# Performance work log

Hardware: AMD Instinct MI355X
Metric: run time of the kernel (lower is better)

## Reference

```python
import jax, jax.numpy as jnp
import numpy as np

F = 192  # channels
HW = 8   # spatial map side


def _conv1x1(x, W, b):
    # x: [B,H,W,C], W: [C,C], b: [C] -- 1x1 conv == per-pixel matmul
    return jnp.einsum('bhwc,cd->bhwd', x, W) + b


def setup_inputs() -> dict:
    key = jax.random.key(0)
    ks = jax.random.split(key, 10)
    B = 4096
    s = 1.0 / np.sqrt(F)
    x = jax.random.normal(ks[0], (B, HW, HW, F), dtype=jnp.float32)
    Wf = jax.random.normal(ks[1], (F, F), dtype=jnp.float32) * s
    bf = jnp.zeros((F,), dtype=jnp.float32)
    Wg = jax.random.normal(ks[2], (F, F), dtype=jnp.float32) * s
    bg = jnp.zeros((F,), dtype=jnp.float32)
    Wh = jax.random.normal(ks[3], (F, F), dtype=jnp.float32) * s
    bh = jnp.zeros((F,), dtype=jnp.float32)
    Wo = jax.random.normal(ks[4], (F, F), dtype=jnp.float32) * s
    bo = jnp.zeros((F,), dtype=jnp.float32)
    # original initializes gamma to zero; use a small nonzero value so the
    # attention branch contributes to the output/gradients
    gamma = jnp.full((1, 1, 1), 0.1, dtype=jnp.float32)
    return {"x": x, "Wf": Wf, "bf": bf, "Wg": Wg, "bg": bg,
            "Wh": Wh, "bh": bh, "Wo": Wo, "bo": bo, "gamma": gamma}


def reference(x, Wf, bf, Wg, bg, Wh, bh, Wo, bo, gamma):
    B = x.shape[0]
    N = HW * HW  # 64 spatial positions
    fx = _conv1x1(x, Wf, bf).reshape(B, N, F)           # queries [B,N,F]
    gx = _conv1x1(x, Wg, bg)                            # [B,H,W,F]
    # tf.transpose to [B,F,H,W] then reshape -> [B,F,N]
    gx = jnp.transpose(gx, (0, 3, 1, 2)).reshape(B, F, N)
    attn = jax.nn.softmax(jnp.einsum('bnf,bfm->bnm', fx, gx), axis=-1)  # [B,N,N]
    hx = _conv1x1(x, Wh, bh).reshape(B, N, F)           # values [B,N,F]
    second = jnp.einsum('bnm,bmf->bnf', attn, hx).reshape(B, HW, HW, F)
    second = _conv1x1(second, Wo, bo)
    return x + gamma * second
```

## Files before the change

### kernel.cpp

```cpp
#include <hip/hip_runtime.h>

#define FCH 192
#define NPOS 64
#define PX 200
#define PH 72
#define PP 72

typedef float f32x4 __attribute__((ext_vector_type(4)));
typedef float float4_t __attribute__((ext_vector_type(4)));
typedef __bf16 bf16x8 __attribute__((ext_vector_type(8)));
typedef unsigned short ushort8_t __attribute__((ext_vector_type(8)));
typedef unsigned short ushort4_t __attribute__((ext_vector_type(4)));

__device__ __forceinline__ unsigned short f2bf(float f) {
  unsigned u = __builtin_bit_cast(unsigned, f);
  u += 0x7fffu + ((u >> 16) & 1u);
  return (unsigned short)(u >> 16);
}

__device__ __forceinline__ bf16x8 frag_ld(const unsigned short* p) {
  return __builtin_bit_cast(bf16x8, *(const ushort8_t*)p);
}

__global__ void prep_weights(const float* __restrict__ Wf, const float* __restrict__ Wg,
                             const float* __restrict__ Wh, const float* __restrict__ Wo,
                             unsigned short* __restrict__ wt) {
  int t = blockIdx.x * blockDim.x + threadIdx.x;
  int n = t % 192;
  int kb = (t / 192) % 48;
  int m = t / (192 * 48);
  const float* W = (m == 0) ? Wf : (m == 1) ? Wg : (m == 2) ? Wh : Wo;
  ushort4_t v;
#pragma unroll
  for (int i = 0; i < 4; ++i) v[i] = f2bf(W[(kb * 4 + i) * 192 + n]);
  *(ushort4_t*)(wt + ((size_t)(m * 192 + n) * 192 + kb * 4)) = v;
}

__global__ __launch_bounds__(256) void spatial_attn(
    const float* __restrict__ x, const unsigned short* __restrict__ wt,
    const float* __restrict__ bfv, const float* __restrict__ bgv,
    const float* __restrict__ bhv, const float* __restrict__ bov,
    const float* __restrict__ gamma_p, float* __restrict__ out) {
  __shared__ unsigned short lds[56832];
  unsigned short* sX  = lds;
  unsigned short* sF  = lds + 12800;
  unsigned short* sG  = lds + 25600;
  unsigned short* sHT = lds + 38400;
  unsigned short* sP  = lds + 52224;
  unsigned short* sS  = lds;

  const int b    = blockIdx.x;
  const int tid  = threadIdx.x;
  const int lane = tid & 63;
  const int w    = tid >> 6;
  const int l15  = lane & 15;
  const int l4   = lane >> 4;

  const float* xb = x + (size_t)b * (NPOS * FCH);

#pragma unroll
  for (int r = 0; r < 12; ++r) {
    int i = tid + 256 * r;
    float4_t v = *(const float4_t*)(xb + (size_t)i * 4);
    int row = (i * 4) / FCH, col = (i * 4) % FCH;
    ushort4_t u;
#pragma unroll
    for (int q = 0; q < 4; ++q) u[q] = f2bf(v[q]);
    *(ushort4_t*)(sX + row * PX + col) = u;
  }
  __syncthreads();

  const unsigned short* WfT = wt;
  const unsigned short* WgT = wt + 36864;
  const unsigned short* WhT = wt + 73728;
  const unsigned short* WoT = wt + 110592;

  auto conv_T = [&](const unsigned short* WT, const float* bias, unsigned short* dst) {
    f32x4 acc[3][4];
#pragma unroll
    for (int mt = 0; mt < 3; ++mt)
#pragma unroll
      for (int nt = 0; nt < 4; ++nt) acc[mt][nt] = f32x4{0.f, 0.f, 0.f, 0.f};
#pragma unroll
    for (int kk = 0; kk < 6; ++kk) {
      int kb = kk * 32 + l4 * 8;
      bf16x8 a[3], bb[4];
#pragma unroll
      for (int mt = 0; mt < 3; ++mt)
        a[mt] = frag_ld(WT + (size_t)(w * 48 + mt * 16 + l15) * 192 + kb);
#pragma unroll
      for (int nt = 0; nt < 4; ++nt)
        bb[nt] = frag_ld(sX + (nt * 16 + l15) * PX + kb);
#pragma unroll
      for (int mt = 0; mt < 3; ++mt)
#pragma unroll
        for (int nt = 0; nt < 4; ++nt)
          acc[mt][nt] = __builtin_amdgcn_mfma_f32_16x16x32_bf16(a[mt], bb[nt], acc[mt][nt], 0, 0, 0);
    }
#pragma unroll
    for (int mt = 0; mt < 3; ++mt) {
      int fb = w * 48 + mt * 16 + l4 * 4;
      float b0 = bias[fb], b1 = bias[fb + 1], b2 = bias[fb + 2], b3 = bias[fb + 3];
#pragma unroll
      for (int nt = 0; nt < 4; ++nt) {
        int n = nt * 16 + l15;
        ushort4_t u;
        u[0] = f2bf(acc[mt][nt][0] + b0);
        u[1] = f2bf(acc[mt][nt][1] + b1);
        u[2] = f2bf(acc[mt][nt][2] + b2);
        u[3] = f2bf(acc[mt][nt][3] + b3);
        *(ushort4_t*)(dst + n * PX + fb) = u;
      }
    }
  };
  conv_T(WfT, bfv, sF);
  conv_T(WgT, bgv, sG);

  {
    f32x4 acc[4][3];
#pragma unroll
    for (int mt = 0; mt < 4; ++mt)
#pragma unroll
      for (int nt = 0; nt < 3; ++nt) acc[mt][nt] = f32x4{0.f, 0.f, 0.f, 0.f};
#pragma unroll
    for (int kk = 0; kk < 6; ++kk) {
      int kb = kk * 32 + l4 * 8;
      bf16x8 a[4], bb[3];
#pragma unroll
      for (int mt = 0; mt < 4; ++mt)
        a[mt] = frag_ld(sX + (mt * 16 + l15) * PX + kb);
#pragma unroll
      for (int nt = 0; nt < 3; ++nt)
        bb[nt] = frag_ld(WhT + (size_t)(w * 48 + nt * 16 + l15) * 192 + kb);
#pragma unroll
      for (int mt = 0; mt < 4; ++mt)
#pragma unroll
        for (int nt = 0; nt < 3; ++nt)
          acc[mt][nt] = __builtin_amdgcn_mfma_f32_16x16x32_bf16(a[mt], bb[nt], acc[mt][nt], 0, 0, 0);
    }
#pragma unroll
    for (int mt = 0; mt < 4; ++mt) {
      int nb = mt * 16 + l4 * 4;
#pragma unroll
      for (int nt = 0; nt < 3; ++nt) {
        int f = w * 48 + nt * 16 + l15;
        float bv = bhv[f];
        ushort4_t u;
#pragma unroll
        for (int j = 0; j < 4; ++j) u[j] = f2bf(acc[mt][nt][j] + bv);
        *(ushort4_t*)(sHT + f * PH + nb) = u;
      }
    }
  }
  __syncthreads();

  {
    f32x4 lg[4];
#pragma unroll
    for (int mt = 0; mt < 4; ++mt) lg[mt] = f32x4{0.f, 0.f, 0.f, 0.f};
#pragma unroll
    for (int kk = 0; kk < 6; ++kk) {
      int kb = kk * 32 + l4 * 8;
      bf16x8 bb = frag_ld(sF + (w * 16 + l15) * PX + kb);
#pragma unroll
      for (int mt = 0; mt < 4; ++mt) {
        bf16x8 a = frag_ld(sG + (mt * 16 + l15) * PX + kb);
        lg[mt] = __builtin_amdgcn_mfma_f32_16x16x32_bf16(a, bb, lg[mt], 0, 0, 0);
      }
    }
    float mx = -1e30f;
#pragma unroll
    for (int mt = 0; mt < 4; ++mt)
#pragma unroll
      for (int j = 0; j < 4; ++j) mx = fmaxf(mx, lg[mt][j]);
    mx = fmaxf(mx, __shfl_xor(mx, 16));
    mx = fmaxf(mx, __shfl_xor(mx, 32));
    float p[4][4];
    float s = 0.f;
#pragma unroll
    for (int mt = 0; mt < 4; ++mt)
#pragma unroll
      for (int j = 0; j < 4; ++j) {
        p[mt][j] = exp2f((lg[mt][j] - mx) * 1.44269504f);
        s += p[mt][j];
      }
    s += __shfl_xor(s, 16);
    s += __shfl_xor(s, 32);
    float inv = 1.0f / s;
    int n = w * 16 + l15;
#pragma unroll
    for (int mt = 0; mt < 4; ++mt) {
      ushort4_t u;
#pragma unroll
      for (int j = 0; j < 4; ++j) u[j] = f2bf(p[mt][j] * inv);
      *(ushort4_t*)(sP + n * PP + mt * 16 + l4 * 4) = u;
    }
  }
  __syncthreads();

  {
    f32x4 acc[3][4];
#pragma unroll
    for (int mt = 0; mt < 3; ++mt)
#pragma unroll
      for (int nt = 0; nt < 4; ++nt) acc[mt][nt] = f32x4{0.f, 0.f, 0.f, 0.f};
#pragma unroll
    for (int kk = 0; kk < 2; ++kk) {
      int kb = kk * 32 + l4 * 8;
      bf16x8 a[3], bb[4];
#pragma unroll
      for (int mt = 0; mt < 3; ++mt)
        a[mt] = frag_ld(sHT + (w * 48 + mt * 16 + l15) * PH + kb);
#pragma unroll
      for (int nt = 0; nt < 4; ++nt)
        bb[nt] = frag_ld(sP + (nt * 16 + l15) * PP + kb);
#pragma unroll
      for (int mt = 0; mt < 3; ++mt)
#pragma unroll
        for (int nt = 0; nt < 4; ++nt)
          acc[mt][nt] = __builtin_amdgcn_mfma_f32_16x16x32_bf16(a[mt], bb[nt], acc[mt][nt], 0, 0, 0);
    }
#pragma unroll
    for (int mt = 0; mt < 3; ++mt) {
      int fb = w * 48 + mt * 16 + l4 * 4;
#pragma unroll
      for (int nt = 0; nt < 4; ++nt) {
        int n = nt * 16 + l15;
        ushort4_t u;
#pragma unroll
        for (int j = 0; j < 4; ++j) u[j] = f2bf(acc[mt][nt][j]);
        *(ushort4_t*)(sS + n * PX + fb) = u;
      }
    }
  }
  __syncthreads();

  {
    f32x4 acc[4][3];
#pragma unroll
    for (int mt = 0; mt < 4; ++mt)
#pragma unroll
      for (int nt = 0; nt < 3; ++nt) acc[mt][nt] = f32x4{0.f, 0.f, 0.f, 0.f};
#pragma unroll
    for (int kk = 0; kk < 6; ++kk) {
      int kb = kk * 32 + l4 * 8;
      bf16x8 a[4], bb[3];
#pragma unroll
      for (int mt = 0; mt < 4; ++mt)
        a[mt] = frag_ld(sS + (mt * 16 + l15) * PX + kb);
#pragma unroll
      for (int nt = 0; nt < 3; ++nt)
        bb[nt] = frag_ld(WoT + (size_t)(w * 48 + nt * 16 + l15) * 192 + kb);
#pragma unroll
      for (int mt = 0; mt < 4; ++mt)
#pragma unroll
        for (int nt = 0; nt < 3; ++nt)
          acc[mt][nt] = __builtin_amdgcn_mfma_f32_16x16x32_bf16(a[mt], bb[nt], acc[mt][nt], 0, 0, 0);
    }
    float gm = gamma_p[0];
    float* ob = out + (size_t)b * (NPOS * FCH);
#pragma unroll
    for (int nt = 0; nt < 3; ++nt) {
      int d = w * 48 + nt * 16 + l15;
      float bv = bov[d];
#pragma unroll
      for (int mt = 0; mt < 4; ++mt) {
        int nb = mt * 16 + l4 * 4;
#pragma unroll
        for (int j = 0; j < 4; ++j) {
          int idx = (nb + j) * FCH + d;
          ob[idx] = xb[idx] + gm * (acc[mt][nt][j] + bv);
        }
      }
    }
  }
}

extern "C" void kernel_launch(void* const* d_in, const int* in_sizes, int n_in,
                              void* d_out, int out_size, void* d_ws, size_t ws_size,
                              hipStream_t stream) {
  const float* x   = (const float*)d_in[0];
  const float* Wf  = (const float*)d_in[1];
  const float* bf_ = (const float*)d_in[2];
  const float* Wg  = (const float*)d_in[3];
  const float* bg_ = (const float*)d_in[4];
  const float* Wh  = (const float*)d_in[5];
  const float* bh_ = (const float*)d_in[6];
  const float* Wo  = (const float*)d_in[7];
  const float* bo_ = (const float*)d_in[8];
  const float* gm  = (const float*)d_in[9];
  unsigned short* wt = (unsigned short*)d_ws;

  prep_weights<<<144, 256, 0, stream>>>(Wf, Wg, Wh, Wo, wt);
  spatial_attn<<<4096, 256, 0, stream>>>(x, wt, bf_, bg_, bh_, bo_, gm, (float*)d_out);
}
```

Before: 561.9 us.

## Fold query/key and value/output weight products to remove two per-pixel GEMMs

Precomputes A = Wf·Wgᵀ and C2 = Wh·Wo, plus bias vectors, in small prep kernels. Bias terms that are constant along the softmax axis are dropped, and bh·Wo+bo is folded into a constant because attention rows sum to one. Per sample the kernel then runs two 64x192x192 projections instead of four. The block grows to 512 threads with smaller LDS to raise occupancy, and the output epilogue becomes a coalesced float4 residual add. Rounding the fused weight matrices to bf16 changes the numerics slightly.

```diff
diff --git a/kernel.cpp b/kernel.cpp
--- a/kernel.cpp
+++ b/kernel.cpp
@@ -17,52 +17,83 @@
   u += 0x7fffu + ((u >> 16) & 1u);
   return (unsigned short)(u >> 16);
 }
-
+__device__ __forceinline__ float bf2f(unsigned short s) {
+  unsigned u = ((unsigned)s) << 16;
+  return __builtin_bit_cast(float, u);
+}
 __device__ __forceinline__ bf16x8 frag_ld(const unsigned short* p) {
   return __builtin_bit_cast(bf16x8, *(const ushort8_t*)p);
 }
 
-__global__ void prep_weights(const float* __restrict__ Wf, const float* __restrict__ Wg,
-                             const float* __restrict__ Wh, const float* __restrict__ Wo,
-                             unsigned short* __restrict__ wt) {
+__global__ void prep_mats(const float* __restrict__ Wf, const float* __restrict__ Wg,
+                          const float* __restrict__ Wh, const float* __restrict__ Wo,
+                          unsigned short* __restrict__ AT, unsigned short* __restrict__ C2T) {
+  __shared__ float col[192];
+  int r = blockIdx.x;
+  int t = threadIdx.x;
+  if (r < 192) {
+    col[t] = Wg[r * 192 + t];
+    __syncthreads();
+    float acc = 0.f;
+#pragma unroll 4
+    for (int f = 0; f < 192; ++f) acc += Wf[t * 192 + f] * col[f];
+    AT[r * 192 + t] = f2bf(acc);
+  } else {
+    int d = r - 192;
+    col[t] = Wo[t * 192 + d];
+    __syncthreads();
+    float acc = 0.f;
+#pragma unroll 4
+    for (int f = 0; f < 192; ++f) acc += Wh[t * 192 + f] * col[f];
+    C2T[d * 192 + t] = f2bf(acc);
+  }
+}
+
+__global__ void prep_vecs(const float* __restrict__ Wg, const float* __restrict__ bfv,
+                          const float* __restrict__ Wo, const float* __restrict__ bhv,
+                          const float* __restrict__ bov,
+                          float* __restrict__ vg, float* __restrict__ c0) {
   int t = blockIdx.x * blockDim.x + threadIdx.x;
-  int n = t % 192;
-  int kb = (t / 192) % 48;
-  int m = t / (192 * 48);
-  const float* W = (m == 0) ? Wf : (m == 1) ? Wg : (m == 2) ? Wh : Wo;
-  ushort4_t v;
-#pragma unroll
-  for (int i = 0; i < 4; ++i) v[i] = f2bf(W[(kb * 4 + i) * 192 + n]);
-  *(ushort4_t*)(wt + ((size_t)(m * 192 + n) * 192 + kb * 4)) = v;
-}
-
-__global__ __launch_bounds__(256) void spatial_attn(
-    const float* __restrict__ x, const unsigned short* __restrict__ wt,
-    const float* __restrict__ bfv, const float* __restrict__ bgv,
-    const float* __restrict__ bhv, const float* __restrict__ bov,
-    const float* __restrict__ gamma_p, float* __restrict__ out) {
-  __shared__ unsigned short lds[56832];
-  unsigned short* sX  = lds;
-  unsigned short* sF  = lds + 12800;
-  unsigned short* sG  = lds + 25600;
-  unsigned short* sHT = lds + 38400;
-  unsigned short* sP  = lds + 52224;
-  unsigned short* sS  = lds;
+  if (t < 192) {
+    float acc = 0.f;
+    for (int f = 0; f < 192; ++f) acc += Wg[t * 192 + f] * bfv[f];
+    vg[t] = acc;
+  } else if (t < 384) {
+    int d = t - 192;
+    float acc = bov[d];
+    for (int f = 0; f < 192; ++f) acc += bhv[f] * Wo[f * 192 + d];
+    c0[d] = acc;
+  }
+}
+
+__global__ __launch_bounds__(512, 4) void spatial_attn(
+    const float* __restrict__ x, const unsigned short* __restrict__ AT,
+    const unsigned short* __restrict__ C2T, const float* __restrict__ vg,
+    const float* __restrict__ c0, const float* __restrict__ gamma_p,
+    float* __restrict__ out) {
+  __shared__ unsigned short lds[31232];
+  unsigned short* sX = lds;
+  unsigned short* sY = lds + 12800;
+  unsigned short* sH = lds + 12800;
+  unsigned short* sP = lds + 26624;
+  unsigned short* sS = lds;
 
   const int b    = blockIdx.x;
   const int tid  = threadIdx.x;
   const int lane = tid & 63;
-  const int w    = tid >> 6;
+  const int wid  = tid >> 6;
   const int l15  = lane & 15;
   const int l4   = lane >> 4;
+  const int wk   = wid & 3;
+  const int wn   = wid >> 2;
 
   const float* xb = x + (size_t)b * (NPOS * FCH);
 
 #pragma unroll
-  for (int r = 0; r < 12; ++r) {
-    int i = tid + 256 * r;
+  for (int r = 0; r < 6; ++r) {
+    int i = tid + 512 * r;
     float4_t v = *(const float4_t*)(xb + (size_t)i * 4);
-    int row = (i * 4) / FCH, col = (i * 4) % FCH;
+    int row = i / 48, col = (i % 48) * 4;
     ushort4_t u;
 #pragma unroll
     for (int q = 0; q < 4; ++q) u[q] = f2bf(v[q]);
@@ -70,101 +101,57 @@
   }
   __syncthreads();
 
-  const unsigned short* WfT = wt;
-  const unsigned short* WgT = wt + 36864;
-  const unsigned short* WhT = wt + 73728;
-  const unsigned short* WoT = wt + 110592;
-
-  auto conv_T = [&](const unsigned short* WT, const float* bias, unsigned short* dst) {
-    f32x4 acc[3][4];
+  {
+    f32x4 acc[3][2];
 #pragma unroll
     for (int mt = 0; mt < 3; ++mt)
 #pragma unroll
-      for (int nt = 0; nt < 4; ++nt) acc[mt][nt] = f32x4{0.f, 0.f, 0.f, 0.f};
+      for (int nt = 0; nt < 2; ++nt) acc[mt][nt] = f32x4{0.f, 0.f, 0.f, 0.f};
 #pragma unroll
     for (int kk = 0; kk < 6; ++kk) {
       int kb = kk * 32 + l4 * 8;
-      bf16x8 a[3], bb[4];
+      bf16x8 a[3], bb[2];
 #pragma unroll
       for (int mt = 0; mt < 3; ++mt)
-        a[mt] = frag_ld(WT + (size_t)(w * 48 + mt * 16 + l15) * 192 + kb);
-#pragma unroll
-      for (int nt = 0; nt < 4; ++nt)
-        bb[nt] = frag_ld(sX + (nt * 16 + l15) * PX + kb);
+        a[mt] = frag_ld(AT + (size_t)(wk * 48 + mt * 16 + l15) * 192 + kb);
+#pragma unroll
+      for (int nt = 0; nt < 2; ++nt)
+        bb[nt] = frag_ld(sX + (wn * 32 + nt * 16 + l15) * PX + kb);
 #pragma unroll
       for (int mt = 0; mt < 3; ++mt)
 #pragma unroll
-        for (int nt = 0; nt < 4; ++nt)
+        for (int nt = 0; nt < 2; ++nt)
           acc[mt][nt] = __builtin_amdgcn_mfma_f32_16x16x32_bf16(a[mt], bb[nt], acc[mt][nt], 0, 0, 0);
     }
 #pragma unroll
     for (int mt = 0; mt < 3; ++mt) {
-      int fb = w * 48 + mt * 16 + l4 * 4;
-      float b0 = bias[fb], b1 = bias[fb + 1], b2 = bias[fb + 2], b3 = bias[fb + 3];
-#pragma unroll
-      for (int nt = 0; nt < 4; ++nt) {
-        int n = nt * 16 + l15;
+      int fb = wk * 48 + mt * 16 + l4 * 4;
+      float b0 = vg[fb], b1 = vg[fb + 1], b2 = vg[fb + 2], b3 = vg[fb + 3];
+#pragma unroll
+      for (int nt = 0; nt < 2; ++nt) {
+        int n = wn * 32 + nt * 16 + l15;
         ushort4_t u;
         u[0] = f2bf(acc[mt][nt][0] + b0);
         u[1] = f2bf(acc[mt][nt][1] + b1);
         u[2] = f2bf(acc[mt][nt][2] + b2);
         u[3] = f2bf(acc[mt][nt][3] + b3);
-        *(ushort4_t*)(dst + n * PX + fb) = u;
-      }
-    }
-  };
-  conv_T(WfT, bfv, sF);
-  conv_T(WgT, bgv, sG);
-
-  {
-    f32x4 acc[4][3];
-#pragma unroll
-    for (int mt = 0; mt < 4; ++mt)
-#pragma unroll
-      for (int nt = 0; nt < 3; ++nt) acc[mt][nt] = f32x4{0.f, 0.f, 0.f, 0.f};
+        *(ushort4_t*)(sY + n * PX + fb) = u;
+      }
+    }
+  }
+  __syncthreads();
+
+  if (wid < 4) {
+    f32x4 lg[4];
+#pragma unroll
+    for (int mt = 0; mt < 4; ++mt) lg[mt] = f32x4{0.f, 0.f, 0.f, 0.f};
 #pragma unroll
     for (int kk = 0; kk < 6; ++kk) {
       int kb = kk * 32 + l4 * 8;
-      bf16x8 a[4], bb[3];
-#pragma unroll
-      for (int mt = 0; mt < 4; ++mt)
-        a[mt] = frag_ld(sX + (mt * 16 + l15) * PX + kb);
-#pragma unroll
-      for (int nt = 0; nt < 3; ++nt)
-        bb[nt] = frag_ld(WhT + (size_t)(w * 48 + nt * 16 + l15) * 192 + kb);
-#pragma unroll
-      for (int mt = 0; mt < 4; ++mt)
-#pragma unroll
-        for (int nt = 0; nt < 3; ++nt)
-          acc[mt][nt] = __builtin_amdgcn_mfma_f32_16x16x32_bf16(a[mt], bb[nt], acc[mt][nt], 0, 0, 0);
-    }
-#pragma unroll
-    for (int mt = 0; mt < 4; ++mt) {
-      int nb = mt * 16 + l4 * 4;
-#pragma unroll
-      for (int nt = 0; nt < 3; ++nt) {
-        int f = w * 48 + nt * 16 + l15;
-        float bv = bhv[f];
-        ushort4_t u;
-#pragma unroll
-        for (int j = 0; j < 4; ++j) u[j] = f2bf(acc[mt][nt][j] + bv);
-        *(ushort4_t*)(sHT + f * PH + nb) = u;
-      }
-    }
-  }
-  __syncthreads();
-
-  {
-    f32x4 lg[4];
-#pragma unroll
-    for (int mt = 0; mt < 4; ++mt) lg[mt] = f32x4{0.f, 0.f, 0.f, 0.f};
-#pragma unroll
-    for (int kk = 0; kk < 6; ++kk) {
-      int kb = kk * 32 + l4 * 8;
-      bf16x8 bb = frag_ld(sF + (w * 16 + l15) * PX + kb);
+      bf16x8 bb = frag_ld(sY + (wid * 16 + l15) * PX + kb);
 #pragma unroll
       for (int mt = 0; mt < 4; ++mt) {
-        bf16x8 a = frag_ld(sG + (mt * 16 + l15) * PX + kb);
+        bf16x8 a = frag_ld(sX + (mt * 16 + l15) * PX + kb);
         lg[mt] = __builtin_amdgcn_mfma_f32_16x16x32_bf16(a, bb, lg[mt], 0, 0, 0);
       }
     }
@@ -187,7 +174,7 @@
     s += __shfl_xor(s, 16);
     s += __shfl_xor(s, 32);
     float inv = 1.0f / s;
-    int n = w * 16 + l15;
+    int n = wid * 16 + l15;
 #pragma unroll
     for (int mt = 0; mt < 4; ++mt) {
       ushort4_t u;
@@ -199,33 +186,71 @@
   __syncthreads();
 
   {
-    f32x4 acc[3][4];
+    f32x4 acc[2][3];
+#pragma unroll
+    for (int mt = 0; mt < 2; ++mt)
+#pragma unroll
+      for (int nt = 0; nt < 3; ++nt) acc[mt][nt] = f32x4{0.f, 0.f, 0.f, 0.f};
+#pragma unroll
+    for (int kk = 0; kk < 6; ++kk) {
+      int kb = kk * 32 + l4 * 8;
+      bf16x8 a[2], bb[3];
+#pragma unroll
+      for (int mt = 0; mt < 2; ++mt)
+        a[mt] = frag_ld(sX + (wn * 32 + mt * 16 + l15) * PX + kb);
+#pragma unroll
+      for (int nt = 0; nt < 3; ++nt)
+        bb[nt] = frag_ld(C2T + (size_t)(wk * 48 + nt * 16 + l15) * 192 + kb);
+#pragma unroll
+      for (int mt = 0; mt < 2; ++mt)
+#pragma unroll
+        for (int nt = 0; nt < 3; ++nt)
+          acc[mt][nt] = __builtin_amdgcn_mfma_f32_16x16x32_bf16(a[mt], bb[nt], acc[mt][nt], 0, 0, 0);
+    }
+#pragma unroll
+    for (int mt = 0; mt < 2; ++mt) {
+      int nb = wn * 32 + mt * 16 + l4 * 4;
+#pragma unroll
+      for (int nt = 0; nt < 3; ++nt) {
+        int d = wk * 48 + nt * 16 + l15;
+        float bv = c0[d];
+        ushort4_t u;
+#pragma unroll
+        for (int j = 0; j < 4; ++j) u[j] = f2bf(acc[mt][nt][j] + bv);
+        *(ushort4_t*)(sH + d * PH + nb) = u;
+      }
+    }
+  }
+  __syncthreads();
+
+  {
+    f32x4 acc[3][2];
 #pragma unroll
     for (int mt = 0; mt < 3; ++mt)
 #pragma unroll
-      for (int nt = 0; nt < 4; ++nt) acc[mt][nt] = f32x4{0.f, 0.f, 0.f, 0.f};
+      for (int nt = 0; nt < 2; ++nt) acc[mt][nt] = f32x4{0.f, 0.f, 0.f, 0.f};
 #pragma unroll
     for (int kk = 0; kk < 2; ++kk) {
       int kb = kk * 32 + l4 * 8;
-      bf16x8 a[3], bb[4];
+      bf16x8 a[3], bb[2];
 #pragma unroll
       for (int mt = 0; mt < 3; ++mt)
-        a[mt] = frag_ld(sHT + (w * 48 + mt * 16 + l15) * PH + kb);
-#pragma unroll
-      for (int nt = 0; nt < 4; ++nt)
-        bb[nt] = frag_ld(sP + (nt * 16 + l15) * PP + kb);
+        a[mt] = frag_ld(sH + (wk * 48 + mt * 16 + l15) * PH + kb);
+#pragma unroll
+      for (int nt = 0; nt < 2; ++nt)
+        bb[nt] = frag_ld(sP + (wn * 32 + nt * 16 + l15) * PP + kb);
 #pragma unroll
       for (int mt = 0; mt < 3; ++mt)
 #pragma unroll
-        for (int nt = 0; nt < 4; ++nt)
+        for (int nt = 0; nt < 2; ++nt)
           acc[mt][nt] = __builtin_amdgcn_mfma_f32_16x16x32_bf16(a[mt], bb[nt], acc[mt][nt], 0, 0, 0);
     }
 #pragma unroll
     for (int mt = 0; mt < 3; ++mt) {
-      int fb = w * 48 + mt * 16 + l4 * 4;
-#pragma unroll
-      for (int nt = 0; nt < 4; ++nt) {
-        int n = nt * 16 + l15;
+      int fb = wk * 48 + mt * 16 + l4 * 4;
+#pragma unroll
+      for (int nt = 0; nt < 2; ++nt) {
+        int n = wn * 32 + nt * 16 + l15;
         ushort4_t u;
 #pragma unroll
         for (int j = 0; j < 4; ++j) u[j] = f2bf(acc[mt][nt][j]);
@@ -236,42 +261,18 @@
   __syncthreads();
 
   {
-    f32x4 acc[4][3];
-#pragma unroll
-    for (int mt = 0; mt < 4; ++mt)
-#pragma unroll
-      for (int nt = 0; nt < 3; ++nt) acc[mt][nt] = f32x4{0.f, 0.f, 0.f, 0.f};
-#pragma unroll
-    for (int kk = 0; kk < 6; ++kk) {
-      int kb = kk * 32 + l4 * 8;
-      bf16x8 a[4], bb[3];
-#pragma unroll
-      for (int mt = 0; mt < 4; ++mt)
-        a[mt] = frag_ld(sS + (mt * 16 + l15) * PX + kb);
-#pragma unroll
-      for (int nt = 0; nt < 3; ++nt)
-        bb[nt] = frag_ld(WoT + (size_t)(w * 48 + nt * 16 + l15) * 192 + kb);
-#pragma unroll
-      for (int mt = 0; mt < 4; ++mt)
-#pragma unroll
-        for (int nt = 0; nt < 3; ++nt)
-          acc[mt][nt] = __builtin_amdgcn_mfma_f32_16x16x32_bf16(a[mt], bb[nt], acc[mt][nt], 0, 0, 0);
-    }
     float gm = gamma_p[0];
     float* ob = out + (size_t)b * (NPOS * FCH);
 #pragma unroll
-    for (int nt = 0; nt < 3; ++nt) {
-      int d = w * 48 + nt * 16 + l15;
-      float bv = bov[d];
-#pragma unroll
-      for (int mt = 0; mt < 4; ++mt) {
-        int nb = mt * 16 + l4 * 4;
-#pragma unroll
-        for (int j = 0; j < 4; ++j) {
-          int idx = (nb + j) * FCH + d;
-          ob[idx] = xb[idx] + gm * (acc[mt][nt][j] + bv);
-        }
-      }
+    for (int r = 0; r < 6; ++r) {
+      int i = tid + 512 * r;
+      int row = i / 48, col = (i % 48) * 4;
+      ushort4_t s4 = *(const ushort4_t*)(sS + row * PX + col);
+      float4_t xv = *(const float4_t*)(xb + (size_t)i * 4);
+      float4_t o;
+#pragma unroll
+      for (int q = 0; q < 4; ++q) o[q] = xv[q] + gm * bf2f(s4[q]);
+      *(float4_t*)(ob + (size_t)i * 4) = o;
     }
   }
 }
@@ -289,8 +290,14 @@
   const float* Wo  = (const float*)d_in[7];
   const float* bo_ = (const float*)d_in[8];
   const float* gm  = (const float*)d_in[9];
-  unsigned short* wt = (unsigned short*)d_ws;
-
-  prep_weights<<<144, 256, 0, stream>>>(Wf, Wg, Wh, Wo, wt);
-  spatial_attn<<<4096, 256, 0, stream>>>(x, wt, bf_, bg_, bh_, bo_, gm, (float*)d_out);
-}
+  (void)bg_;
+
+  unsigned short* AT  = (unsigned short*)d_ws;
+  unsigned short* C2T = AT + 36864;
+  float* vg = (float*)(C2T + 36864);
+  float* c0 = vg + 192;
+
+  prep_mats<<<384, 192, 0, stream>>>(Wf, Wg, Wh, Wo, AT, C2T);
+  prep_vecs<<<2, 192, 0, stream>>>(Wg, bf_, Wo, bh_, bo_, vg, c0);
+  spatial_attn<<<4096, 512, 0, stream>>>(x, AT, C2T, vg, c0, gm, (float*)d_out);
+}
```

After: 476.4 us. -15.2%, faster.
